# Kernel tuning notes

Measured on AMD Instinct MI355X. Metric: run time of the kernel, lower is better.

The kernel has to match this reference:

```python
import jax, jax.numpy as jnp
import numpy as np

KY, KX = 3, 3  # kernel_size from init_kwargs


def setup_inputs() -> dict:
    key = jax.random.key(0)
    x = jax.random.normal(key, (8, 64, 256, 256), dtype=jnp.float32)
    return {"x": x}


def reference(x):
    # NMS: mask = x > max over 3x3 replicate-padded neighborhood EXCLUDING center.
    # Note: the torch conv kernel zeroes the center row, so the center output
    # channel is all zeros and the max implicitly includes 0 — we replicate that
    # by initializing the running max to zeros.
    ky, kx = KY, KX
    py, px = (ky - 1) // 2, (kx - 1) // 2
    H, W = x.shape[-2], x.shape[-1]
    xp = jnp.pad(x, ((0, 0), (0, 0), (py, py), (px, px)), mode='edge')  # replicate pad
    numel = ky * kx
    center = numel // 2
    max_non_center = jnp.zeros_like(x)  # zeroed-center channel participates in max
    for i in range(numel):  # fixed small kernel window, unrolled (8 shifts)
        if i == center:
            continue
        dy, dx = divmod(i, kx)
        max_non_center = jnp.maximum(max_non_center, xp[..., dy:dy + H, dx:dx + W])
    mask = x > max_non_center
    return x * mask.astype(x.dtype)
```

## Files before the change

kernel.cpp:

```cpp
#include <hip/hip_runtime.h>


#define NMS_H 256
#define NMS_W 256
#define PLANE (NMS_H * NMS_W)
#define GRID_BLOCKS 8192

typedef float f4_t __attribute__((ext_vector_type(4)));

struct HV {
    float4 h;
    float4 lr;
};

__device__ __forceinline__ HV rowmax(const float4 v, const int tx) {
    float l = __shfl_up(v.w, 1, 64);
    float r = __shfl_down(v.x, 1, 64);
    if (tx == 0)  l = v.x;
    if (tx == 63) r = v.w;
    HV o;
    o.h.x = fmaxf(l,   fmaxf(v.x, v.y));
    o.h.y = fmaxf(v.x, fmaxf(v.y, v.z));
    o.h.z = fmaxf(v.y, fmaxf(v.z, v.w));
    o.h.w = fmaxf(v.z, fmaxf(v.w, r));
    o.lr.x = fmaxf(l,   v.y);
    o.lr.y = fmaxf(v.x, v.z);
    o.lr.z = fmaxf(v.y, v.w);
    o.lr.w = fmaxf(v.z, r);
    return o;
}

__device__ __forceinline__ f4_t nmspick(const float4 vc, const float4 ha,
                                        const float4 hb, const float4 lrc) {
    f4_t o;
    float m;
    m = fmaxf(0.0f, fmaxf(fmaxf(ha.x, hb.x), lrc.x)); o.x = (vc.x > m) ? vc.x : 0.0f;
    m = fmaxf(0.0f, fmaxf(fmaxf(ha.y, hb.y), lrc.y)); o.y = (vc.y > m) ? vc.y : 0.0f;
    m = fmaxf(0.0f, fmaxf(fmaxf(ha.z, hb.z), lrc.z)); o.z = (vc.z > m) ? vc.z : 0.0f;
    m = fmaxf(0.0f, fmaxf(fmaxf(ha.w, hb.w), lrc.w)); o.w = (vc.w > m) ? vc.w : 0.0f;
    return o;
}

__global__ __launch_bounds__(256, 4) void nms2d_kernel(const float* __restrict__ x,
                                                       float* __restrict__ out) {
    const int blk     = blockIdx.x;
    const int logical = (blk >> 3) + (blk & 7) * (GRID_BLOCKS / 8);

    const int plane_idx = logical >> 4;
    const int rg        = logical & 15;
    const int tx        = threadIdx.x & 63;
    const int R         = rg * 16 + (threadIdx.x >> 6) * 4;
    const int col4      = tx * 4;

    const float* pl = x + (size_t)plane_idx * PLANE + col4;

    const int rm = max(R - 1, 0);
    const int rp = min(R + 4, NMS_H - 1);
    const float4 vm = *reinterpret_cast<const float4*>(pl + rm      * NMS_W);
    const float4 v0 = *reinterpret_cast<const float4*>(pl + (R + 0) * NMS_W);
    const float4 v1 = *reinterpret_cast<const float4*>(pl + (R + 1) * NMS_W);
    const float4 v2 = *reinterpret_cast<const float4*>(pl + (R + 2) * NMS_W);
    const float4 v3 = *reinterpret_cast<const float4*>(pl + (R + 3) * NMS_W);
    const float4 vp = *reinterpret_cast<const float4*>(pl + rp      * NMS_W);

    const HV hm = rowmax(vm, tx);
    const HV h0 = rowmax(v0, tx);
    const HV h1 = rowmax(v1, tx);
    const HV h2 = rowmax(v2, tx);
    const HV h3 = rowmax(v3, tx);
    const HV hp = rowmax(vp, tx);

    float* po = out + (size_t)plane_idx * PLANE + col4;
    *reinterpret_cast<f4_t*>(po + (R + 0) * NMS_W) = nmspick(v0, hm.h, h1.h, h0.lr);
    *reinterpret_cast<f4_t*>(po + (R + 1) * NMS_W) = nmspick(v1, h0.h, h2.h, h1.lr);
    *reinterpret_cast<f4_t*>(po + (R + 2) * NMS_W) = nmspick(v2, h1.h, h3.h, h2.lr);
    *reinterpret_cast<f4_t*>(po + (R + 3) * NMS_W) = nmspick(v3, h2.h, hp.h, h3.lr);
}

extern "C" void kernel_launch(void* const* d_in, const int* in_sizes, int n_in,
                              void* d_out, int out_size, void* d_ws, size_t ws_size,
                              hipStream_t stream) {
    const float* x = (const float*)d_in[0];
    float* out = (float*)d_out;

    dim3 block(256);
    dim3 grid(GRID_BLOCKS);
    nms2d_kernel<<<grid, block, 0, stream>>>(x, out);
}
```

Measured before the change: 229.7 us.

## Process 16 rows per wave with rolling halo reuse and software-pipelined loads

Each wavefront now handles 16 consecutive rows instead of 4, carrying the previous row's horizontal max and center values in registers. This cuts the halo reads per output row from 6/4 to 18/16. The next group of rows is loaded before the current group is computed, giving a simple software pipeline. The grid shrinks by a factor of four, which raises register pressure and leaves fewer waves to hide memory latency.

```diff
diff --git a/kernel.cpp b/kernel.cpp
--- a/kernel.cpp
+++ b/kernel.cpp
@@ -4,7 +4,7 @@
 #define NMS_H 256
 #define NMS_W 256
 #define PLANE (NMS_H * NMS_W)
-#define GRID_BLOCKS 8192
+#define GRID_BLOCKS 2048
 
 typedef float f4_t __attribute__((ext_vector_type(4)));
 
@@ -41,40 +41,70 @@
     return o;
 }
 
+__device__ __forceinline__ void nms_step(const float4 v1, const float4 v2,
+                                         const float4 v3, const float4 v4,
+                                         float4& vr, float4& hA, HV& hC,
+                                         float* __restrict__ po, const int r,
+                                         const int tx) {
+    const HV h1 = rowmax(v1, tx);
+    const HV h2 = rowmax(v2, tx);
+    const HV h3 = rowmax(v3, tx);
+    const HV h4 = rowmax(v4, tx);
+    *reinterpret_cast<f4_t*>(po + (r + 0) * NMS_W) = nmspick(vr, hA,   h1.h, hC.lr);
+    *reinterpret_cast<f4_t*>(po + (r + 1) * NMS_W) = nmspick(v1, hC.h, h2.h, h1.lr);
+    *reinterpret_cast<f4_t*>(po + (r + 2) * NMS_W) = nmspick(v2, h1.h, h3.h, h2.lr);
+    *reinterpret_cast<f4_t*>(po + (r + 3) * NMS_W) = nmspick(v3, h2.h, h4.h, h3.lr);
+    vr = v4;
+    hA = h3.h;
+    hC = h4;
+}
+
 __global__ __launch_bounds__(256, 4) void nms2d_kernel(const float* __restrict__ x,
                                                        float* __restrict__ out) {
     const int blk     = blockIdx.x;
     const int logical = (blk >> 3) + (blk & 7) * (GRID_BLOCKS / 8);
 
-    const int plane_idx = logical >> 4;
-    const int rg        = logical & 15;
+    const int plane_idx = logical >> 2;
+    const int quarter   = logical & 3;
+    const int w         = threadIdx.x >> 6;
     const int tx        = threadIdx.x & 63;
-    const int R         = rg * 16 + (threadIdx.x >> 6) * 4;
+    const int R0        = quarter * 64 + w * 16;
     const int col4      = tx * 4;
 
-    const float* pl = x + (size_t)plane_idx * PLANE + col4;
+    const float* pl = x   + (size_t)plane_idx * PLANE + col4;
+    float*       po = out + (size_t)plane_idx * PLANE + col4;
 
-    const int rm = max(R - 1, 0);
-    const int rp = min(R + 4, NMS_H - 1);
-    const float4 vm = *reinterpret_cast<const float4*>(pl + rm      * NMS_W);
-    const float4 v0 = *reinterpret_cast<const float4*>(pl + (R + 0) * NMS_W);
-    const float4 v1 = *reinterpret_cast<const float4*>(pl + (R + 1) * NMS_W);
-    const float4 v2 = *reinterpret_cast<const float4*>(pl + (R + 2) * NMS_W);
-    const float4 v3 = *reinterpret_cast<const float4*>(pl + (R + 3) * NMS_W);
-    const float4 vp = *reinterpret_cast<const float4*>(pl + rp      * NMS_W);
+    const int rm = max(R0 - 1, 0);
+    const float4 vm = *reinterpret_cast<const float4*>(pl + rm       * NMS_W);
+    float4 vr       = *reinterpret_cast<const float4*>(pl + R0       * NMS_W);
+    const float4 a1 = *reinterpret_cast<const float4*>(pl + (R0 + 1) * NMS_W);
+    const float4 a2 = *reinterpret_cast<const float4*>(pl + (R0 + 2) * NMS_W);
+    const float4 a3 = *reinterpret_cast<const float4*>(pl + (R0 + 3) * NMS_W);
+    const float4 a4 = *reinterpret_cast<const float4*>(pl + (R0 + 4) * NMS_W);
 
-    const HV hm = rowmax(vm, tx);
-    const HV h0 = rowmax(v0, tx);
-    const HV h1 = rowmax(v1, tx);
-    const HV h2 = rowmax(v2, tx);
-    const HV h3 = rowmax(v3, tx);
-    const HV hp = rowmax(vp, tx);
+    float4 hA = rowmax(vm, tx).h;
+    HV     hC = rowmax(vr, tx);
 
-    float* po = out + (size_t)plane_idx * PLANE + col4;
-    *reinterpret_cast<f4_t*>(po + (R + 0) * NMS_W) = nmspick(v0, hm.h, h1.h, h0.lr);
-    *reinterpret_cast<f4_t*>(po + (R + 1) * NMS_W) = nmspick(v1, h0.h, h2.h, h1.lr);
-    *reinterpret_cast<f4_t*>(po + (R + 2) * NMS_W) = nmspick(v2, h1.h, h3.h, h2.lr);
-    *reinterpret_cast<f4_t*>(po + (R + 3) * NMS_W) = nmspick(v3, h2.h, hp.h, h3.lr);
+    const float4 b1 = *reinterpret_cast<const float4*>(pl + (R0 + 5) * NMS_W);
+    const float4 b2 = *reinterpret_cast<const float4*>(pl + (R0 + 6) * NMS_W);
+    const float4 b3 = *reinterpret_cast<const float4*>(pl + (R0 + 7) * NMS_W);
+    const float4 b4 = *reinterpret_cast<const float4*>(pl + (R0 + 8) * NMS_W);
+    nms_step(a1, a2, a3, a4, vr, hA, hC, po, R0, tx);
+
+    const float4 c1 = *reinterpret_cast<const float4*>(pl + (R0 +  9) * NMS_W);
+    const float4 c2 = *reinterpret_cast<const float4*>(pl + (R0 + 10) * NMS_W);
+    const float4 c3 = *reinterpret_cast<const float4*>(pl + (R0 + 11) * NMS_W);
+    const float4 c4 = *reinterpret_cast<const float4*>(pl + (R0 + 12) * NMS_W);
+    nms_step(b1, b2, b3, b4, vr, hA, hC, po, R0 + 4, tx);
+
+    const int rl = min(R0 + 16, NMS_H - 1);
+    const float4 d1 = *reinterpret_cast<const float4*>(pl + (R0 + 13) * NMS_W);
+    const float4 d2 = *reinterpret_cast<const float4*>(pl + (R0 + 14) * NMS_W);
+    const float4 d3 = *reinterpret_cast<const float4*>(pl + (R0 + 15) * NMS_W);
+    const float4 d4 = *reinterpret_cast<const float4*>(pl + rl        * NMS_W);
+    nms_step(c1, c2, c3, c4, vr, hA, hC, po, R0 + 8, tx);
+
+    nms_step(d1, d2, d3, d4, vr, hA, hC, po, R0 + 12, tx);
 }
 
 extern "C" void kernel_launch(void* const* d_in, const int* in_sizes, int n_in,
```

After: 242.4 us. 1.06x slower.
